# Optimization experiments

Hardware: AMD Instinct MI355X
Metric: run time of the kernel (lower is better)

The kernel has to match this reference:

```python
import jax, jax.numpy as jnp
import numpy as np

N_NODES = 100000
N_EDGES = 3200000
N_GRAPHS = 128
IN_DIM, HID, OUT = 128, 64, 128


def gcn_conv(x, W, b, src, dst, n_nodes):
    """PyG GCNConv: add self-loops, symmetric deg^-1/2 normalization, scatter-add."""
    xw = x @ W  # [N, H]
    ones = jnp.ones(src.shape[0], dtype=x.dtype)
    deg = jax.ops.segment_sum(ones, dst, num_segments=n_nodes) + 1.0  # +1 self loop
    dinv = jax.lax.rsqrt(deg)
    norm = dinv[src] * dinv[dst]  # [E]
    agg = jax.ops.segment_sum(xw[src] * norm[:, None], dst, num_segments=n_nodes)
    # self-loop contribution: norm = dinv * dinv = 1/deg
    return agg + xw * (1.0 / deg)[:, None] + b


def global_mean_pool(x, batch, n_graphs):
    sums = jax.ops.segment_sum(x, batch, num_segments=n_graphs)
    cnts = jax.ops.segment_sum(jnp.ones(x.shape[0], dtype=x.dtype), batch, num_segments=n_graphs)
    return sums / jnp.maximum(cnts, 1.0)[:, None]


def setup_inputs() -> dict:
    key = jax.random.key(0)
    ks = jax.random.split(key, 9)
    x = jax.random.normal(ks[0], (N_NODES, IN_DIM), dtype=jnp.float32)
    edge_index = jax.random.randint(ks[1], (2, N_EDGES), 0, N_NODES, dtype=jnp.int64)
    batch = jnp.sort(jax.random.randint(ks[2], (N_NODES,), 0, N_GRAPHS, dtype=jnp.int64))
    def glorot(k, shp):
        lim = float(np.sqrt(6.0 / (shp[0] + shp[1])))
        return jax.random.uniform(k, shp, dtype=jnp.float32, minval=-lim, maxval=lim)
    return {
        "x": x,
        "edge_index": edge_index,
        "batch": batch,
        "W1": glorot(ks[3], (IN_DIM, HID)),
        "b1": jnp.zeros((HID,), jnp.float32),
        "W2": glorot(ks[4], (HID, HID)),
        "b2": jnp.zeros((HID,), jnp.float32),
        "Wl": glorot(ks[5], (HID, OUT)),
        "bl": jnp.zeros((OUT,), jnp.float32),
    }


def reference(x, edge_index, batch, W1, b1, W2, b2, Wl, bl):
    src, dst = edge_index[0], edge_index[1]
    h = jax.nn.relu(gcn_conv(x, W1, b1, src, dst, N_NODES))
    h = jax.nn.relu(gcn_conv(h, W2, b2, src, dst, N_NODES))
    g = global_mean_pool(h, batch, N_GRAPHS)  # [G, HID]
    return g @ Wl + bl  # [G, OUT]
```

## Files before the change

kernel.cpp:

```cpp
#include <hip/hip_runtime.h>
#include <math.h>

#define N_NODES    100000
#define N_EDGES    3200000
#define N_GRAPHS   128
#define IN_DIM     128
#define HID        64
#define OUT_DIM    128
#define NBKT       391
#define BIN_BLOCKS 512
#define E_PER_BIN  6250

typedef unsigned short ushort_t;

__device__ __forceinline__ float bf2f(ushort_t u) {
    return __uint_as_float(((unsigned int)u) << 16);
}
__device__ __forceinline__ ushort_t f2bf(float f) {
    unsigned int u = __float_as_uint(f);
    u += 0x7FFFu + ((u >> 16) & 1u);
    return (ushort_t)(u >> 16);
}

__global__ __launch_bounds__(256) void k_bkt_hist(const int* __restrict__ dst,
                                                  int* __restrict__ bkt_cnt) {
    __shared__ int hist[NBKT];
    int t = threadIdx.x;
    for (int b = t; b < NBKT; b += 256) hist[b] = 0;
    __syncthreads();
    int e0 = blockIdx.x * E_PER_BIN;
    for (int e = e0 + t; e < e0 + E_PER_BIN; e += 256)
        atomicAdd(&hist[dst[e] >> 8], 1);
    __syncthreads();
    for (int b = t; b < NBKT; b += 256) {
        int h = hist[b];
        if (h) atomicAdd(&bkt_cnt[b], h);
    }
}

__global__ void k_scan_bkt(const int* __restrict__ bkt_cnt,
                           int* __restrict__ bkt_ptr, int* __restrict__ bkt_cur) {
    __shared__ int s[512];
    int t = threadIdx.x;
    int v = (t < NBKT) ? bkt_cnt[t] : 0;
    s[t] = v; __syncthreads();
    for (int d = 1; d < 512; d <<= 1) {
        int add = (t >= d) ? s[t - d] : 0;
        __syncthreads();
        s[t] += add;
        __syncthreads();
    }
    int excl = s[t] - v;
    if (t <= NBKT) bkt_ptr[t] = excl;
    if (t < NBKT)  bkt_cur[t] = excl;
}

__global__ __launch_bounds__(256) void k_bin(const int* __restrict__ src,
                                             const int* __restrict__ dst,
                                             int* __restrict__ bkt_cursor,
                                             unsigned int* __restrict__ recs) {
    __shared__ int hist[NBKT];
    __shared__ int base[NBKT];
    int t = threadIdx.x;
    int e0 = blockIdx.x * E_PER_BIN;
    int e1 = e0 + E_PER_BIN;
    for (int b = t; b < NBKT; b += 256) hist[b] = 0;
    __syncthreads();
    for (int e = e0 + t; e < e1; e += 256)
        atomicAdd(&hist[dst[e] >> 8], 1);
    __syncthreads();
    for (int b = t; b < NBKT; b += 256) {
        int h = hist[b];
        base[b] = h ? atomicAdd(&bkt_cursor[b], h) : 0;
        hist[b] = 0;
    }
    __syncthreads();
    for (int e = e0 + t; e < e1; e += 256) {
        int d = dst[e];
        int b = d >> 8;
        int pos = base[b] + atomicAdd(&hist[b], 1);
        recs[pos] = ((unsigned int)src[e] << 8) | (unsigned int)(d & 255);
    }
}

__global__ __launch_bounds__(256) void k_csrA(const unsigned int* __restrict__ recs,
                                              const int* __restrict__ bkt_ptr,
                                              int* __restrict__ row_ptr,
                                              float* __restrict__ dinv,
                                              int* __restrict__ csr_src) {
    __shared__ int lcnt[256];
    __shared__ int s[256];
    __shared__ int lcur[256];
    int b = blockIdx.x, t = threadIdx.x;
    int start = bkt_ptr[b], end = bkt_ptr[b + 1];
    lcnt[t] = 0;
    __syncthreads();
    for (int i = start + t; i < end; i += 256)
        atomicAdd(&lcnt[recs[i] & 255u], 1);
    __syncthreads();
    int v = lcnt[t];
    s[t] = v; __syncthreads();
    for (int d = 1; d < 256; d <<= 1) {
        int add = (t >= d) ? s[t - d] : 0;
        __syncthreads();
        s[t] += add;
        __syncthreads();
    }
    int excl = s[t] - v;
    int n = b * 256 + t;
    if (n <= N_NODES) row_ptr[n] = start + excl;
    if (n < N_NODES)  dinv[n] = 1.0f / sqrtf((float)v + 1.0f);
    lcur[t] = start + excl;
    __syncthreads();
    for (int i = start + t; i < end; i += 256) {
        unsigned int r = recs[i];
        int p = atomicAdd(&lcur[r & 255u], 1);
        csr_src[p] = (int)(r >> 8);
    }
}

template <int K>
__global__ __launch_bounds__(256) void k_gemm(const float* __restrict__ X,
                                              const float* __restrict__ W,
                                              const float* __restrict__ dinv,
                                              ushort_t* __restrict__ Ybf, int nrows) {
    __shared__ float Ws[K * 64];
    __shared__ float Xs[16][K];
    int t = threadIdx.x;
    for (int i = t; i < K * 64; i += 256) Ws[i] = W[i];
    int row0 = blockIdx.x * 16;
    for (int i = t; i < 16 * K; i += 256) {
        int r = i / K, k = i % K;
        int gr = row0 + r;
        Xs[r][k] = (gr < nrows) ? X[gr * K + k] : 0.0f;
    }
    __syncthreads();
    int c = t & 63, rg = t >> 6;
    float acc[4] = {0.f, 0.f, 0.f, 0.f};
#pragma unroll 4
    for (int k = 0; k < K; ++k) {
        float w = Ws[k * 64 + c];
#pragma unroll
        for (int i = 0; i < 4; ++i) acc[i] += Xs[rg * 4 + i][k] * w;
    }
#pragma unroll
    for (int i = 0; i < 4; ++i) {
        int gr = row0 + rg * 4 + i;
        if (gr < nrows) Ybf[(size_t)gr * 64 + c] = f2bf(dinv[gr] * acc[i]);
    }
}

__global__ __launch_bounds__(256) void k_gather(const ushort_t* __restrict__ xwp,
                                                const float* __restrict__ dinv,
                                                const int* __restrict__ row_ptr,
                                                const int* __restrict__ csr_src,
                                                const float* __restrict__ bias,
                                                float* __restrict__ hout) {
    int wave = threadIdx.x >> 6;
    int lane = threadIdx.x & 63;
    int n = blockIdx.x * 4 + wave;
    if (n >= N_NODES) return;
    int sub = lane >> 4, c4 = lane & 15;
    int start = row_ptr[n], end = row_ptr[n + 1];
    float ax = 0.f, ay = 0.f, az = 0.f, aw = 0.f;
    int i = start + sub;
    for (; i + 4 < end; i += 8) {
        int s0 = csr_src[i];
        int s1 = csr_src[i + 4];
        const ushort4 v0 = *(const ushort4*)(xwp + (size_t)s0 * 64 + c4 * 4);
        const ushort4 v1 = *(const ushort4*)(xwp + (size_t)s1 * 64 + c4 * 4);
        ax += bf2f(v0.x) + bf2f(v1.x); ay += bf2f(v0.y) + bf2f(v1.y);
        az += bf2f(v0.z) + bf2f(v1.z); aw += bf2f(v0.w) + bf2f(v1.w);
    }
    if (i < end) {
        int s0 = csr_src[i];
        const ushort4 v = *(const ushort4*)(xwp + (size_t)s0 * 64 + c4 * 4);
        ax += bf2f(v.x); ay += bf2f(v.y); az += bf2f(v.z); aw += bf2f(v.w);
    }
    ax += __shfl_xor(ax, 16, 64); ay += __shfl_xor(ay, 16, 64);
    az += __shfl_xor(az, 16, 64); aw += __shfl_xor(aw, 16, 64);
    ax += __shfl_xor(ax, 32, 64); ay += __shfl_xor(ay, 32, 64);
    az += __shfl_xor(az, 32, 64); aw += __shfl_xor(aw, 32, 64);
    if (sub == 0) {
        float dn = dinv[n];
        const ushort4 xn = *(const ushort4*)(xwp + (size_t)n * 64 + c4 * 4);
        const float4 bv = *(const float4*)(bias + c4 * 4);
        float4 r;
        r.x = fmaxf(dn * (ax + bf2f(xn.x)) + bv.x, 0.f);
        r.y = fmaxf(dn * (ay + bf2f(xn.y)) + bv.y, 0.f);
        r.z = fmaxf(dn * (az + bf2f(xn.z)) + bv.z, 0.f);
        r.w = fmaxf(dn * (aw + bf2f(xn.w)) + bv.w, 0.f);
        *(float4*)(hout + (size_t)n * 64 + c4 * 4) = r;
    }
}

__device__ __forceinline__ int lower_bound(const int* __restrict__ a, int n, int key) {
    int lo = 0, hi = n;
    while (lo < hi) {
        int mid = (lo + hi) >> 1;
        if (a[mid] < key) lo = mid + 1; else hi = mid;
    }
    return lo;
}

__global__ __launch_bounds__(1024) void k_pool(const float* __restrict__ h,
                                               const int* __restrict__ batch,
                                               float* __restrict__ g) {
    int b = blockIdx.x;
    int t = threadIdx.x, c = t & 63, rg = t >> 6;
    __shared__ float s[16][64];
    int start = lower_bound(batch, N_NODES, b);
    int end   = lower_bound(batch, N_NODES, b + 1);
    float sum = 0.f;
    for (int n = start + rg; n < end; n += 16) sum += h[(size_t)n * 64 + c];
    s[rg][c] = sum;
    __syncthreads();
    if (rg == 0) {
        float tot = 0.f;
#pragma unroll
        for (int k = 0; k < 16; ++k) tot += s[k][c];
        float cntf = (float)(end - start);
        g[b * 64 + c] = tot / fmaxf(cntf, 1.0f);
    }
}

__global__ void k_final(const float* __restrict__ g, const float* __restrict__ Wl,
                        const float* __restrict__ bl, float* __restrict__ out) {
    __shared__ float gs[64];
    int row = blockIdx.x, c = threadIdx.x;
    if (c < 64) gs[c] = g[row * 64 + c];
    __syncthreads();
    float acc = bl[c];
#pragma unroll
    for (int k = 0; k < 64; ++k) acc += gs[k] * Wl[k * 128 + c];
    out[row * 128 + c] = acc;
}

extern "C" void kernel_launch(void* const* d_in, const int* in_sizes, int n_in,
                              void* d_out, int out_size, void* d_ws, size_t ws_size,
                              hipStream_t stream) {
    const float* x    = (const float*)d_in[0];
    const int*   ei   = (const int*)d_in[1];
    const int*   batch= (const int*)d_in[2];
    const float* W1   = (const float*)d_in[3];
    const float* b1   = (const float*)d_in[4];
    const float* W2   = (const float*)d_in[5];
    const float* b2   = (const float*)d_in[6];
    const float* Wl   = (const float*)d_in[7];
    const float* bl   = (const float*)d_in[8];
    float* out = (float*)d_out;

    const int* src = ei;
    const int* dst = ei + N_EDGES;

    char* base = (char*)d_ws;
    float*        dinv     = (float*)(base + 0);
    int*          row_ptr  = (int*)  (base + 400128);
    int*          bkt_cnt  = (int*)  (base + 800256);
    int*          bkt_ptr  = (int*)  (base + 802304);
    int*          bkt_cur  = (int*)  (base + 804352);
    int*          csr_src  = (int*)  (base + 806400);
    ushort_t*     xwp      = (ushort_t*)(base + 13606400);
    float*        h        = (float*)(base + 26406400);
    float*        g        = (float*)(base + 52006400);
    unsigned int* recs     = (unsigned int*)xwp;

    hipMemsetAsync(bkt_cnt, 0, NBKT * sizeof(int), stream);
    k_bkt_hist<<<BIN_BLOCKS, 256, 0, stream>>>(dst, bkt_cnt);
    k_scan_bkt<<<1, 512, 0, stream>>>(bkt_cnt, bkt_ptr, bkt_cur);
    k_bin     <<<BIN_BLOCKS, 256, 0, stream>>>(src, dst, bkt_cur, recs);
    k_csrA    <<<NBKT, 256, 0, stream>>>(recs, bkt_ptr, row_ptr, dinv, csr_src);

    k_gemm<IN_DIM><<<(N_NODES + 15) / 16, 256, 0, stream>>>(x, W1, dinv, xwp, N_NODES);
    k_gather<<<(N_NODES + 3) / 4, 256, 0, stream>>>(xwp, dinv, row_ptr, csr_src, b1, h);

    k_gemm<HID><<<(N_NODES + 15) / 16, 256, 0, stream>>>(h, W2, dinv, xwp, N_NODES);
    k_gather<<<(N_NODES + 3) / 4, 256, 0, stream>>>(xwp, dinv, row_ptr, csr_src, b2, h);

    k_pool <<<N_GRAPHS, 1024, 0, stream>>>(h, batch, g);
    k_final<<<N_GRAPHS, 128, 0, stream>>>(g, Wl, bl, out);
}
```

Before: 341.6 us.

## Sort CSR neighbours in LDS, register-tile GEMM, widen gather loads

```diff
diff --git a/kernel.cpp b/kernel.cpp
--- a/kernel.cpp
+++ b/kernel.cpp
@@ -10,12 +10,10 @@
 #define NBKT       391
 #define BIN_BLOCKS 512
 #define E_PER_BIN  6250
+#define LMAX       10240
 
 typedef unsigned short ushort_t;
 
-__device__ __forceinline__ float bf2f(ushort_t u) {
-    return __uint_as_float(((unsigned int)u) << 16);
-}
 __device__ __forceinline__ ushort_t f2bf(float f) {
     unsigned int u = __float_as_uint(f);
     u += 0x7FFFu + ((u >> 16) & 1u);
@@ -91,8 +89,10 @@
     __shared__ int lcnt[256];
     __shared__ int s[256];
     __shared__ int lcur[256];
+    __shared__ int lrecs[LMAX];
     int b = blockIdx.x, t = threadIdx.x;
     int start = bkt_ptr[b], end = bkt_ptr[b + 1];
+    int total = end - start;
     lcnt[t] = 0;
     __syncthreads();
     for (int i = start + t; i < end; i += 256)
@@ -110,12 +110,31 @@
     int n = b * 256 + t;
     if (n <= N_NODES) row_ptr[n] = start + excl;
     if (n < N_NODES)  dinv[n] = 1.0f / sqrtf((float)v + 1.0f);
-    lcur[t] = start + excl;
-    __syncthreads();
-    for (int i = start + t; i < end; i += 256) {
-        unsigned int r = recs[i];
-        int p = atomicAdd(&lcur[r & 255u], 1);
-        csr_src[p] = (int)(r >> 8);
+    lcur[t] = excl;
+    __syncthreads();
+    if (total <= LMAX) {
+        for (int i = start + t; i < end; i += 256) {
+            unsigned int r = recs[i];
+            int p = atomicAdd(&lcur[r & 255u], 1);
+            lrecs[p] = (int)(r >> 8);
+        }
+        __syncthreads();
+        int ls = excl, le = excl + v;
+        for (int i = ls + 1; i < le; ++i) {
+            int key = lrecs[i];
+            int j = i - 1;
+            while (j >= ls && lrecs[j] > key) { lrecs[j + 1] = lrecs[j]; --j; }
+            lrecs[j + 1] = key;
+        }
+        __syncthreads();
+        for (int i = t; i < total; i += 256)
+            csr_src[start + i] = lrecs[i];
+    } else {
+        for (int i = start + t; i < end; i += 256) {
+            unsigned int r = recs[i];
+            int p = atomicAdd(&lcur[r & 255u], 1);
+            csr_src[start + p] = (int)(r >> 8);
+        }
     }
 }
 
@@ -124,29 +143,56 @@
                                               const float* __restrict__ W,
                                               const float* __restrict__ dinv,
                                               ushort_t* __restrict__ Ybf, int nrows) {
-    __shared__ float Ws[K * 64];
-    __shared__ float Xs[16][K];
+    __shared__ float Xs[64][65];
+    __shared__ float Ws[64][64];
     int t = threadIdx.x;
-    for (int i = t; i < K * 64; i += 256) Ws[i] = W[i];
-    int row0 = blockIdx.x * 16;
-    for (int i = t; i < 16 * K; i += 256) {
-        int r = i / K, k = i % K;
-        int gr = row0 + r;
-        Xs[r][k] = (gr < nrows) ? X[gr * K + k] : 0.0f;
-    }
-    __syncthreads();
-    int c = t & 63, rg = t >> 6;
-    float acc[4] = {0.f, 0.f, 0.f, 0.f};
-#pragma unroll 4
-    for (int k = 0; k < K; ++k) {
-        float w = Ws[k * 64 + c];
-#pragma unroll
-        for (int i = 0; i < 4; ++i) acc[i] += Xs[rg * 4 + i][k] * w;
+    int row0 = blockIdx.x * 64;
+    int tc = t & 15, tr = t >> 4;
+    int c0 = tc * 4, r0 = tr * 4;
+    float acc[4][4] = {};
+    for (int kc = 0; kc < K; kc += 64) {
+        __syncthreads();
+#pragma unroll
+        for (int i = 0; i < 16; ++i) {
+            int e = i * 256 + t;
+            int r = e >> 6, k = e & 63;
+            int gr = row0 + r;
+            Xs[r][k] = (gr < nrows) ? X[(size_t)gr * K + kc + k] : 0.0f;
+        }
+#pragma unroll
+        for (int i = 0; i < 16; ++i) {
+            int e = i * 256 + t;
+            int k = e >> 6, c = e & 63;
+            Ws[k][c] = W[(size_t)(kc + k) * 64 + c];
+        }
+        __syncthreads();
+#pragma unroll 8
+        for (int k = 0; k < 64; ++k) {
+            float xv[4];
+#pragma unroll
+            for (int i = 0; i < 4; ++i) xv[i] = Xs[r0 + i][k];
+            const float4 w4 = *(const float4*)&Ws[k][c0];
+#pragma unroll
+            for (int i = 0; i < 4; ++i) {
+                acc[i][0] += xv[i] * w4.x;
+                acc[i][1] += xv[i] * w4.y;
+                acc[i][2] += xv[i] * w4.z;
+                acc[i][3] += xv[i] * w4.w;
+            }
+        }
     }
 #pragma unroll
     for (int i = 0; i < 4; ++i) {
-        int gr = row0 + rg * 4 + i;
-        if (gr < nrows) Ybf[(size_t)gr * 64 + c] = f2bf(dinv[gr] * acc[i]);
+        int gr = row0 + r0 + i;
+        if (gr < nrows) {
+            float dn = dinv[gr];
+            ushort4 o;
+            o.x = f2bf(dn * acc[i][0]);
+            o.y = f2bf(dn * acc[i][1]);
+            o.z = f2bf(dn * acc[i][2]);
+            o.w = f2bf(dn * acc[i][3]);
+            *(ushort4*)(Ybf + (size_t)gr * 64 + c0) = o;
+        }
     }
 }
 
@@ -160,37 +206,62 @@
     int lane = threadIdx.x & 63;
     int n = blockIdx.x * 4 + wave;
     if (n >= N_NODES) return;
-    int sub = lane >> 4, c4 = lane & 15;
+    int sub = lane >> 3, c8 = (lane & 7) * 8;
     int start = row_ptr[n], end = row_ptr[n + 1];
-    float ax = 0.f, ay = 0.f, az = 0.f, aw = 0.f;
+    float a[8] = {0.f, 0.f, 0.f, 0.f, 0.f, 0.f, 0.f, 0.f};
     int i = start + sub;
-    for (; i + 4 < end; i += 8) {
+    for (; i + 8 < end; i += 16) {
         int s0 = csr_src[i];
-        int s1 = csr_src[i + 4];
-        const ushort4 v0 = *(const ushort4*)(xwp + (size_t)s0 * 64 + c4 * 4);
-        const ushort4 v1 = *(const ushort4*)(xwp + (size_t)s1 * 64 + c4 * 4);
-        ax += bf2f(v0.x) + bf2f(v1.x); ay += bf2f(v0.y) + bf2f(v1.y);
-        az += bf2f(v0.z) + bf2f(v1.z); aw += bf2f(v0.w) + bf2f(v1.w);
+        int s1 = csr_src[i + 8];
+        const uint4 v0 = *(const uint4*)(xwp + (size_t)s0 * 64 + c8);
+        const uint4 v1 = *(const uint4*)(xwp + (size_t)s1 * 64 + c8);
+        a[0] += __uint_as_float(v0.x << 16) + __uint_as_float(v1.x << 16);
+        a[1] += __uint_as_float(v0.x & 0xFFFF0000u) + __uint_as_float(v1.x & 0xFFFF0000u);
+        a[2] += __uint_as_float(v0.y << 16) + __uint_as_float(v1.y << 16);
+        a[3] += __uint_as_float(v0.y & 0xFFFF0000u) + __uint_as_float(v1.y & 0xFFFF0000u);
+        a[4] += __uint_as_float(v0.z << 16) + __uint_as_float(v1.z << 16);
+        a[5] += __uint_as_float(v0.z & 0xFFFF0000u) + __uint_as_float(v1.z & 0xFFFF0000u);
+        a[6] += __uint_as_float(v0.w << 16) + __uint_as_float(v1.w << 16);
+        a[7] += __uint_as_float(v0.w & 0xFFFF0000u) + __uint_as_float(v1.w & 0xFFFF0000u);
     }
     if (i < end) {
         int s0 = csr_src[i];
-        const ushort4 v = *(const ushort4*)(xwp + (size_t)s0 * 64 + c4 * 4);
-        ax += bf2f(v.x); ay += bf2f(v.y); az += bf2f(v.z); aw += bf2f(v.w);
-    }
-    ax += __shfl_xor(ax, 16, 64); ay += __shfl_xor(ay, 16, 64);
-    az += __shfl_xor(az, 16, 64); aw += __shfl_xor(aw, 16, 64);
-    ax += __shfl_xor(ax, 32, 64); ay += __shfl_xor(ay, 32, 64);
-    az += __shfl_xor(az, 32, 64); aw += __shfl_xor(aw, 32, 64);
+        const uint4 v = *(const uint4*)(xwp + (size_t)s0 * 64 + c8);
+        a[0] += __uint_as_float(v.x << 16);
+        a[1] += __uint_as_float(v.x & 0xFFFF0000u);
+        a[2] += __uint_as_float(v.y << 16);
+        a[3] += __uint_as_float(v.y & 0xFFFF0000u);
+        a[4] += __uint_as_float(v.z << 16);
+        a[5] += __uint_as_float(v.z & 0xFFFF0000u);
+        a[6] += __uint_as_float(v.w << 16);
+        a[7] += __uint_as_float(v.w & 0xFFFF0000u);
+    }
+#pragma unroll
+    for (int off = 8; off < 64; off <<= 1) {
+#pragma unroll
+        for (int j = 0; j < 8; ++j) a[j] += __shfl_xor(a[j], off, 64);
+    }
     if (sub == 0) {
         float dn = dinv[n];
-        const ushort4 xn = *(const ushort4*)(xwp + (size_t)n * 64 + c4 * 4);
-        const float4 bv = *(const float4*)(bias + c4 * 4);
-        float4 r;
-        r.x = fmaxf(dn * (ax + bf2f(xn.x)) + bv.x, 0.f);
-        r.y = fmaxf(dn * (ay + bf2f(xn.y)) + bv.y, 0.f);
-        r.z = fmaxf(dn * (az + bf2f(xn.z)) + bv.z, 0.f);
-        r.w = fmaxf(dn * (aw + bf2f(xn.w)) + bv.w, 0.f);
-        *(float4*)(hout + (size_t)n * 64 + c4 * 4) = r;
+        const uint4 xn = *(const uint4*)(xwp + (size_t)n * 64 + c8);
+        float xnf[8];
+        xnf[0] = __uint_as_float(xn.x << 16); xnf[1] = __uint_as_float(xn.x & 0xFFFF0000u);
+        xnf[2] = __uint_as_float(xn.y << 16); xnf[3] = __uint_as_float(xn.y & 0xFFFF0000u);
+        xnf[4] = __uint_as_float(xn.z << 16); xnf[5] = __uint_as_float(xn.z & 0xFFFF0000u);
+        xnf[6] = __uint_as_float(xn.w << 16); xnf[7] = __uint_as_float(xn.w & 0xFFFF0000u);
+        float4 b0 = *(const float4*)(bias + c8);
+        float4 b1 = *(const float4*)(bias + c8 + 4);
+        float4 r0, r1;
+        r0.x = fmaxf(dn * (a[0] + xnf[0]) + b0.x, 0.f);
+        r0.y = fmaxf(dn * (a[1] + xnf[1]) + b0.y, 0.f);
+        r0.z = fmaxf(dn * (a[2] + xnf[2]) + b0.z, 0.f);
+        r0.w = fmaxf(dn * (a[3] + xnf[3]) + b0.w, 0.f);
+        r1.x = fmaxf(dn * (a[4] + xnf[4]) + b1.x, 0.f);
+        r1.y = fmaxf(dn * (a[5] + xnf[5]) + b1.y, 0.f);
+        r1.z = fmaxf(dn * (a[6] + xnf[6]) + b1.z, 0.f);
+        r1.w = fmaxf(dn * (a[7] + xnf[7]) + b1.w, 0.f);
+        *(float4*)(hout + (size_t)n * 64 + c8)     = r0;
+        *(float4*)(hout + (size_t)n * 64 + c8 + 4) = r1;
     }
 }
 
@@ -260,10 +331,10 @@
     int*          bkt_ptr  = (int*)  (base + 802304);
     int*          bkt_cur  = (int*)  (base + 804352);
     int*          csr_src  = (int*)  (base + 806400);
-    ushort_t*     xwp      = (ushort_t*)(base + 13606400);
-    float*        h        = (float*)(base + 26406400);
-    float*        g        = (float*)(base + 52006400);
-    unsigned int* recs     = (unsigned int*)xwp;
+    unsigned int* recs     = (unsigned int*)(base + 13606400);
+    ushort_t*     xwp      = (ushort_t*)(base + 26406400);
+    float*        h        = (float*)(base + 39206400);
+    float*        g        = (float*)(base + 64806400);
 
     hipMemsetAsync(bkt_cnt, 0, NBKT * sizeof(int), stream);
     k_bkt_hist<<<BIN_BLOCKS, 256, 0, stream>>>(dst, bkt_cnt);
@@ -271,10 +342,12 @@
     k_bin     <<<BIN_BLOCKS, 256, 0, stream>>>(src, dst, bkt_cur, recs);
     k_csrA    <<<NBKT, 256, 0, stream>>>(recs, bkt_ptr, row_ptr, dinv, csr_src);
 
-    k_gemm<IN_DIM><<<(N_NODES + 15) / 16, 256, 0, stream>>>(x, W1, dinv, xwp, N_NODES);
+    const int GEMM_GRID = (N_NODES + 63) / 64;
+
+    k_gemm<IN_DIM><<<GEMM_GRID, 256, 0, stream>>>(x, W1, dinv, xwp, N_NODES);
     k_gather<<<(N_NODES + 3) / 4, 256, 0, stream>>>(xwp, dinv, row_ptr, csr_src, b1, h);
 
-    k_gemm<HID><<<(N_NODES + 15) / 16, 256, 0, stream>>>(h, W2, dinv, xwp, N_NODES);
+    k_gemm<HID><<<GEMM_GRID, 256, 0, stream>>>(h, W2, dinv, xwp, N_NODES);
     k_gather<<<(N_NODES + 3) / 4, 256, 0, stream>>>(xwp, dinv, row_ptr, csr_src, b2, h);
 
     k_pool <<<N_GRAPHS, 1024, 0, stream>>>(h, batch, g);
```

Result: slower. 399.3 us (+16.9%).
